# Kernel optimization log

Hardware: AMD Instinct MI355X
Metric: run time of the kernel (lower is better)

Reference implementation:

```python
import jax, jax.numpy as jnp
from jax import lax
import numpy as np

WIN = 7            # skimage structural_similarity default win_size
K1, K2 = 0.01, 0.03
DATA_RANGE = 1.0


def _mean_filter_valid(x, win):
    k = jnp.ones((1, 1, win, win), x.dtype) / (win * win)
    y = lax.conv_general_dilated(x[:, None], k, (1, 1), 'VALID')
    return y[:, 0]


def ssim_loss(img1, img2):
    # img1, img2: (B, H, W); skimage-style SSIM, mean over batch of (1 - ssim)
    f = lambda z: _mean_filter_valid(z, WIN)
    NP = WIN * WIN
    cov_norm = NP / (NP - 1.0)  # unbiased estimator, as in skimage
    ux, uy = f(img1), f(img2)
    uxx, uyy, uxy = f(img1 * img1), f(img2 * img2), f(img1 * img2)
    vx = cov_norm * (uxx - ux * ux)
    vy = cov_norm * (uyy - uy * uy)
    vxy = cov_norm * (uxy - ux * uy)
    C1 = (K1 * DATA_RANGE) ** 2
    C2 = (K2 * DATA_RANGE) ** 2
    S = ((2 * ux * uy + C1) * (2 * vxy + C2)) / ((ux * ux + uy * uy + C1) * (vx + vy + C2))
    return jnp.mean(1.0 - jnp.mean(S, axis=(1, 2)))


def conv2d_same(x, w, b):
    # x: (B, Cin, H, W), w: (Cout, Cin, 3, 3)
    y = lax.conv_general_dilated(x, w, (1, 1), 'SAME')
    return y + b[None, :, None, None]


def maxpool2(x):
    return lax.reduce_window(x, -jnp.inf, lax.max, (1, 1, 2, 2), (1, 1, 2, 2), 'VALID')


def features(x, w1, b1, w2, b2, w3, b3, w4, b4):
    h = jax.nn.relu(conv2d_same(x, w1, b1))
    h = jax.nn.relu(conv2d_same(h, w2, b2))
    h = maxpool2(h)
    h = jax.nn.relu(conv2d_same(h, w3, b3))
    h = jax.nn.relu(conv2d_same(h, w4, b4))
    return h


def _conv_init(key, cout, cin, k=3):
    # torch Conv2d default init: U(-s, s), s = 1/sqrt(cin*k*k)
    kw, kb = jax.random.split(key)
    s = 1.0 / np.sqrt(cin * k * k)
    w = jax.random.uniform(kw, (cout, cin, k, k), jnp.float32, -s, s)
    b = jax.random.uniform(kb, (cout,), jnp.float32, -s, s)
    return w, b


def setup_inputs() -> dict:
    key = jax.random.key(0)
    ks = jax.random.split(key, 6)
    B, H, W = 8, 256, 256
    sr = jax.random.uniform(ks[0], (B, 1, H, W), jnp.float32)
    hr = jax.random.uniform(ks[1], (B, 1, H, W), jnp.float32)
    w1, b1 = _conv_init(ks[2], 64, 1)
    w2, b2 = _conv_init(ks[3], 128, 64)
    w3, b3 = _conv_init(ks[4], 256, 128)
    w4, b4 = _conv_init(ks[5], 256, 256)
    return {"sr": sr, "hr": hr, "w1": w1, "b1": b1, "w2": w2, "b2": b2,
            "w3": w3, "b3": b3, "w4": w4, "b4": b4}


def reference(sr, hr, w1, b1, w2, b2, w3, b3, w4, b4):
    mse_weight, ssim_weight, perceptual_weight = 1.0, 0.5, 0.1
    mse = jnp.mean((sr - hr) ** 2)
    # torch detaches before SSIM (numpy round-trip) -> no gradient through SSIM
    ssim_l = ssim_loss(lax.stop_gradient(sr[:, 0]), lax.stop_gradient(hr[:, 0]))
    sr_f = features(sr, w1, b1, w2, b2, w3, b3, w4, b4)
    hr_f = features(hr, w1, b1, w2, b2, w3, b3, w4, b4)
    perceptual = jnp.mean((sr_f - hr_f) ** 2)
    total = mse_weight * mse + ssim_weight * ssim_l + perceptual_weight * perceptual
    return total, mse, ssim_l, perceptual
```

## Files before the change

kernel.cpp:

```cpp
#include <hip/hip_runtime.h>
#include <hip/hip_bf16.h>

typedef __hip_bfloat16 bf16;
typedef unsigned char u8;
typedef __attribute__((ext_vector_type(4))) float f32x4;
typedef __attribute__((ext_vector_type(8))) int i32x8;
typedef __attribute__((ext_vector_type(4))) unsigned int u32x4;

struct L4 { long a, b, c, d; };
struct U2 { u32x4 x, y; };

typedef __attribute__((address_space(3))) unsigned int lds_uint;
typedef __attribute__((address_space(1))) const unsigned int g_uint;
__device__ inline void gload_lds16(const void* g, void* l) {
    __builtin_amdgcn_global_load_lds((g_uint*)g, (lds_uint*)l, 16, 0, 0);
}

__device__ inline void block_reduce_atomic(float v, float* dst) {
    #pragma unroll
    for (int o = 32; o > 0; o >>= 1) v += __shfl_down(v, o, 64);
    __shared__ float ws[8];
    const int lane = threadIdx.x & 63;
    const int wid  = threadIdx.x >> 6;
    if (lane == 0) ws[wid] = v;
    __syncthreads();
    if (threadIdx.x == 0) {
        float s = 0.f;
        const int nw = (blockDim.x + 63) >> 6;
        for (int i = 0; i < nw; ++i) s += ws[i];
        atomicAdd(dst, s);
    }
}

__global__ void prep_loss_kernel(
    const float* __restrict__ w2, u8* __restrict__ wb2,
    const float* __restrict__ w3, u8* __restrict__ wb3,
    const float* __restrict__ w4, u8* __restrict__ wb4,
    const float* __restrict__ x, const float* __restrict__ y,
    float* __restrict__ accs) {
    const int blk = blockIdx.x;
    if (blk < 3744) {
        const float* w; u8* wb; int CIN, CO, idx;
        if (blk < 288)       { w = w2; wb = wb2; CIN = 64;  CO = 128; idx = blk * 256 + threadIdx.x; }
        else if (blk < 1440) { w = w3; wb = wb3; CIN = 128; CO = 256; idx = (blk - 288) * 256 + threadIdx.x; }
        else                 { w = w4; wb = wb4; CIN = 256; CO = 256; idx = (blk - 1440) * 256 + threadIdx.x; }
        int n = CO * 9 * CIN;
        if (idx >= n) return;
        int t = idx % 9;
        int rest = idx / 9;
        int ci = rest % CIN;
        int co = rest / CIN;
        float v = w[idx];
        int p = ci >> 5, c32 = ci & 31;
        size_t off = (size_t)p * 288 * CO;
        if (t < 8) off += (((size_t)t * 2 + (c32 >> 4)) * CO + co) * 16 + (c32 & 15);
        else       off += 256 * (size_t)CO + (((size_t)(c32 >> 4)) * CO + co) * 16 + (c32 & 15);
        int r = __builtin_amdgcn_cvt_pk_fp8_f32(v, v, 0, false);
        wb[off] = (u8)(r & 0xff);
        return;
    }
    const int lb = blk - 3744;
    float val = 0.f;
    float* dst;
    if (lb < 1960) {
        dst = accs + 1;
        const int b = lb / 245;
        const int t = (lb - b * 245) * 256 + threadIdx.x;
        if (t < 250 * 250) {
            const int i = t / 250, j = t - (t / 250) * 250;
            const float* xp = x + (size_t)b * 65536;
            const float* yp = y + (size_t)b * 65536;
            float sx = 0.f, sy = 0.f, sxx = 0.f, syy = 0.f, sxy = 0.f;
            #pragma unroll
            for (int dy = 0; dy < 7; ++dy) {
                const float* xr = xp + (size_t)(i + dy) * 256 + j;
                const float* yr = yp + (size_t)(i + dy) * 256 + j;
                #pragma unroll
                for (int dx = 0; dx < 7; ++dx) {
                    float a = xr[dx], c = yr[dx];
                    sx += a; sy += c;
                    sxx += a * a; syy += c * c; sxy += a * c;
                }
            }
            const float inv = 1.f / 49.f;
            const float cn  = 49.f / 48.f;
            float ux = sx * inv, uy = sy * inv;
            float vx  = cn * (sxx * inv - ux * ux);
            float vy  = cn * (syy * inv - uy * uy);
            float vxy = cn * (sxy * inv - ux * uy);
            const float C1 = 1e-4f, C2 = 9e-4f;
            val = ((2.f * ux * uy + C1) * (2.f * vxy + C2)) /
                  ((ux * ux + uy * uy + C1) * (vx + vy + C2));
        }
    } else {
        dst = accs + 0;
        int i = (lb - 1960) * 256 + threadIdx.x;
        float4 a = ((const float4*)x)[i];
        float4 b = ((const float4*)y)[i];
        float d0 = a.x - b.x, d1 = a.y - b.y, d2 = a.z - b.z, d3 = a.w - b.w;
        val = d0 * d0 + d1 * d1 + d2 * d2 + d3 * d3;
    }
    block_reduce_atomic(val, dst);
}

__global__ void finalize_kernel(const float* __restrict__ accs, float* __restrict__ out) {
    if (threadIdx.x == 0) {
        float mse    = accs[0] * (1.f / 524288.f);
        float ssim_l = 1.f - accs[1] * (1.f / 500000.f);
        float perc   = accs[2] * (1.f / 33554432.f);
        out[0] = mse + 0.5f * ssim_l + 0.1f * perc;
        out[1] = mse;
        out[2] = ssim_l;
        out[3] = perc;
    }
}

__global__ __launch_bounds__(256) void conv1_kernel(
    const float* __restrict__ sr, const float* __restrict__ hr, int nb, int b0,
    const float* __restrict__ w, const float* __restrict__ bias,
    u8* __restrict__ out) {
    const int H = 256, W = 256;
    const int img = blockIdx.y;
    const float* in = (img < nb) ? (sr + (size_t)(b0 + img) * 65536)
                                 : (hr + (size_t)(b0 + img - nb) * 65536);
    int px = blockIdx.x * 256 + threadIdx.x;
    int y = px >> 8, x = px & 255;
    float p[9];
    #pragma unroll
    for (int dy = 0; dy < 3; ++dy)
        #pragma unroll
        for (int dx = 0; dx < 3; ++dx) {
            int gy = y + dy - 1, gx = x + dx - 1;
            float v = 0.f;
            if ((unsigned)gy < (unsigned)H && (unsigned)gx < (unsigned)W)
                v = in[(size_t)gy * W + gx];
            p[dy * 3 + dx] = v;
        }
    #pragma unroll
    for (int g = 0; g < 8; ++g) {
        float v[8];
        #pragma unroll
        for (int c = 0; c < 8; ++c) {
            int co = g * 8 + c;
            float a = bias[co];
            #pragma unroll
            for (int k = 0; k < 9; ++k) a += w[co * 9 + k] * p[k];
            v[c] = fmaxf(a, 0.f);
        }
        uint2 o;
        int r;
        r = __builtin_amdgcn_cvt_pk_fp8_f32(v[0], v[1], 0, false);
        o.x = __builtin_amdgcn_cvt_pk_fp8_f32(v[2], v[3], r, true);
        r = __builtin_amdgcn_cvt_pk_fp8_f32(v[4], v[5], 0, false);
        o.y = __builtin_amdgcn_cvt_pk_fp8_f32(v[6], v[7], r, true);
        *(uint2*)(out + (((size_t)img * 8 + g) * 65536 + px) * 8) = o;
    }
}

#define BUF_SZ   32768
#define N_ACT_CH 720
#define N_CHUNK  1872
#define WT_BOFF  11520

__global__ __launch_bounds__(256, 2) void conv2_ss(
    const u8* __restrict__ in, const u8* __restrict__ wb,
    const float* __restrict__ bias, u8* __restrict__ out,
    const float* __restrict__ zbuf) {
    const int H = 256, W = 256, CO = 128;
    const size_t HW = 65536;
    const int tid  = threadIdx.x;
    const int lane = tid & 63;
    const int wn   = tid >> 6;
    const int xl = lane & 15;
    const int kq = lane >> 4;
    const int x0 = blockIdx.x * 16;
    const int y0 = blockIdx.y * 16;
    const int img = blockIdx.z >> 1;
    const int co0 = (blockIdx.z & 1) << 6;

    __shared__ __align__(16) char smem[59904];

    f32x4 acc[4][4];
    #pragma unroll
    for (int m = 0; m < 4; ++m)
        #pragma unroll
        for (int n = 0; n < 4; ++n) acc[m][n] = (f32x4){0.f, 0.f, 0.f, 0.f};

    const u8* inp = in + (size_t)img * 8 * HW * 8;

    {
        char* d = smem + tid * 16;
        #pragma unroll
        for (int i = 0; i < 15; ++i) {
            int c = tid + i * 256;
            if (c >= 2 * N_CHUNK) break;
            int ph = (c >= N_CHUNK) ? 1 : 0;
            int c2 = c - ph * N_CHUNK;
            const char* src = (const char*)zbuf;
            if (c2 < N_ACT_CH) {
                int g = c2 / 180, r = c2 - g * 180;
                int row = r / 10, pp = r - row * 10;
                int gy = y0 - 1 + row, colb = x0 - 2 + pp * 2;
                if ((unsigned)gy < (unsigned)H && (unsigned)colb < (unsigned)(W - 1))
                    src = (const char*)(inp + (((size_t)(g + ph * 4)) * HW +
                                              (size_t)gy * W + colb) * 8);
            } else {
                int c3 = c2 - N_ACT_CH;
                size_t o;
                if (c3 < 1024) {
                    int gt = c3 >> 6, co = c3 & 63;
                    o = ((size_t)gt * CO + co0 + co) * 16;
                } else {
                    int c4 = c3 - 1024;
                    int q = c4 >> 6, co = c4 & 63;
                    o = 256 * (size_t)CO + ((size_t)q * CO + co0 + co) * 16;
                }
                src = (const char*)(wb + (size_t)ph * 288 * CO + o);
            }
            gload_lds16(src, d + i * 4096);
        }
    }

    int mxo[2];
    #pragma unroll
    for (int g = 0; g < 2; ++g) {
        int t = g * 4 + kq;
        int dy = t / 3, dx = t - dy * 3;
        mxo[g] = (dy * 20 + dx) * 8;
    }
    const int abase = ((wn * 4) * 20 + xl + 1) * 8;
    const int awmx  = WT_BOFF + kq * 2048 + xl * 16;
    const int aw8   = WT_BOFF + 16384 + (kq >> 1) * 1024 + xl * 16 + (kq & 1) * 8;
    const int ab8   = kq * 2880 + abase + (2 * 20 + 2) * 8;

    __syncthreads();

    #pragma unroll
    for (int p = 0; p < 2; ++p) {
        const char* base = smem + p * 29952;
        #pragma unroll
        for (int g = 0; g < 2; ++g) {
            i32x8 A[4];
            #pragma unroll
            for (int mt = 0; mt < 4; ++mt) {
                const char* pa = base + awmx + g * 8192 + mt * 256;
                U2 u{*(const u32x4*)pa, *(const u32x4*)(pa + 1024)};
                A[mt] = __builtin_bit_cast(i32x8, u);
            }
            #pragma unroll
            for (int nt = 0; nt < 4; ++nt) {
                const char* pb = base + abase + mxo[g] + nt * 160;
                L4 l{*(const long*)pb, *(const long*)(pb + 2880),
                     *(const long*)(pb + 5760), *(const long*)(pb + 8640)};
                i32x8 B = __builtin_bit_cast(i32x8, l);
                #pragma unroll
                for (int mt = 0; mt < 4; ++mt)
                    acc[mt][nt] = __builtin_amdgcn_mfma_scale_f32_16x16x128_f8f6f4(
                        A[mt], B, acc[mt][nt], 0, 0,
                        0, 0x7F7F7F7F, 0, 0x7F7F7F7F);
            }
        }
        {
            long A8[4], B8[4];
            #pragma unroll
            for (int mt = 0; mt < 4; ++mt)
                A8[mt] = *(const long*)(base + aw8 + mt * 256);
            #pragma unroll
            for (int nt = 0; nt < 4; ++nt)
                B8[nt] = *(const long*)(base + ab8 + nt * 160);
            #pragma unroll
            for (int mt = 0; mt < 4; ++mt)
                #pragma unroll
                for (int nt = 0; nt < 4; ++nt)
                    acc[mt][nt] = __builtin_amdgcn_mfma_f32_16x16x32_fp8_fp8(
                        A8[mt], B8[nt], acc[mt][nt], 0, 0, 0);
        }
    }

    const int Hp = H >> 1, Wp = W >> 1;
    const size_t HWp = (size_t)Hp * Wp;
    #pragma unroll
    for (int j = 0; j < 2; ++j) {
        const int py = (y0 + wn * 4 + 2 * j) >> 1;
        const int px = (x0 + xl) >> 1;
        #pragma unroll
        for (int mt = 0; mt < 4; ++mt) {
            const int cb = co0 + mt * 16 + kq * 4;
            const f32x4 bv = *(const f32x4*)(bias + cb);
            float v[4];
            #pragma unroll
            for (int r = 0; r < 4; ++r) {
                float a = acc[mt][2 * j][r] + bv[r];
                float b = acc[mt][2 * j + 1][r] + bv[r];
                float m = fmaxf(a, b);
                m = fmaxf(m, __shfl_xor(m, 1));
                v[r] = fmaxf(m, 0.f);
            }
            if (!(lane & 1)) {
                int w0 = __builtin_amdgcn_cvt_pk_fp8_f32(v[0], v[1], 0, false);
                w0 = __builtin_amdgcn_cvt_pk_fp8_f32(v[2], v[3], w0, true);
                *(int*)(out + (((size_t)img * (CO >> 3) + (cb >> 3)) * HWp +
                               (size_t)py * Wp + px) * 8 + (cb & 7)) = w0;
            }
        }
    }
}

template <int CIN, int EPI>
__global__ __launch_bounds__(256, 2) void conv_mx(
    const u8* __restrict__ in, const u8* __restrict__ wb,
    const float* __restrict__ bias, u8* __restrict__ out,
    int H, int W, int CO,
    const float* __restrict__ zbuf) {
    const int tid  = threadIdx.x;
    const int lane = tid & 63;
    const int wn   = tid >> 6;
    const int xl = lane & 15;
    const int kq = lane >> 4;
    const int x0 = blockIdx.x * 16;
    const int y0 = blockIdx.y * 16;
    const int ngrp = CO >> 6;
    const int img = blockIdx.z / ngrp;
    const int co0 = (blockIdx.z - img * ngrp) << 6;

    __shared__ __align__(16) char smem[2 * BUF_SZ];

    f32x4 acc[4][4];
    #pragma unroll
    for (int m = 0; m < 4; ++m)
        #pragma unroll
        for (int n = 0; n < 4; ++n) acc[m][n] = (f32x4){0.f, 0.f, 0.f, 0.f};

    const size_t HW = (size_t)H * W;
    const u8* inp = in + (size_t)img * (CIN >> 3) * HW * 8;

    const char* srcp[8];
    long adv[8];
    #pragma unroll
    for (int i = 0; i < 8; ++i) {
        int c = tid + i * 256;
        srcp[i] = (const char*)zbuf;
        adv[i] = 0;
        if (c < N_ACT_CH) {
            int g = c / 180, r = c - g * 180;
            int row = r / 10, pp = r - row * 10;
            int gy = y0 - 1 + row, colb = x0 - 2 + pp * 2;
            if ((unsigned)gy < (unsigned)H && (unsigned)colb < (unsigned)(W - 1)) {
                srcp[i] = (const char*)(inp + ((size_t)g * HW + (size_t)gy * W + colb) * 8);
                adv[i] = 4 * HW * 8;
            }
        } else if (c < N_CHUNK) {
            int c2 = c - N_ACT_CH;
            size_t o;
            if (c2 < 1024) {
                int gt = c2 >> 6, co = c2 & 63;
                o = ((size_t)gt * CO + co0 + co) * 16;
            } else {
                int c3 = c2 - 1024;
                int q = c3 >> 6, co = c3 & 63;
                o = 256 * (size_t)CO + ((size_t)q * CO + co0 + co) * 16;
            }
            srcp[i] = (const char*)(wb + o);
            adv[i] = 288 * (size_t)CO;
        }
    }

    int mxo[2];
    #pragma unroll
    for (int g = 0; g < 2; ++g) {
        int t = g * 4 + kq;
        int dy = t / 3, dx = t - dy * 3;
        mxo[g] = (dy * 20 + dx) * 8;
    }
    const int abase = ((wn * 4) * 20 + xl + 1) * 8;
    const int awmx  = WT_BOFF + kq * 2048 + xl * 16;
    const int aw8   = WT_BOFF + 16384 + (kq >> 1) * 1024 + xl * 16 + (kq & 1) * 8;
    const int ab8   = kq * 2880 + abase + (2 * 20 + 2) * 8;

    const int P = CIN / 32;

    {
        char* d = smem + tid * 16;
        #pragma unroll
        for (int i = 0; i < 8; ++i) {
            gload_lds16(srcp[i], d + i * 4096);
            srcp[i] += adv[i];
        }
    }

    for (int p = 0; p < P; ++p) {
        __syncthreads();
        if (p + 1 < P) {
            char* d = smem + ((p + 1) & 1) * BUF_SZ + tid * 16;
            #pragma unroll
            for (int i = 0; i < 8; ++i) {
                gload_lds16(srcp[i], d + i * 4096);
                srcp[i] += adv[i];
            }
        }
        const char* base = smem + (p & 1) * BUF_SZ;
        #pragma unroll
        for (int g = 0; g < 2; ++g) {
            i32x8 A[4];
            #pragma unroll
            for (int mt = 0; mt < 4; ++mt) {
                const char* pa = base + awmx + g * 8192 + mt * 256;
                U2 u{*(const u32x4*)pa, *(const u32x4*)(pa + 1024)};
                A[mt] = __builtin_bit_cast(i32x8, u);
            }
            #pragma unroll
            for (int nt = 0; nt < 4; ++nt) {
                const char* pb = base + abase + mxo[g] + nt * 160;
                L4 l{*(const long*)pb, *(const long*)(pb + 2880),
                     *(const long*)(pb + 5760), *(const long*)(pb + 8640)};
                i32x8 B = __builtin_bit_cast(i32x8, l);
                #pragma unroll
                for (int mt = 0; mt < 4; ++mt)
                    acc[mt][nt] = __builtin_amdgcn_mfma_scale_f32_16x16x128_f8f6f4(
                        A[mt], B, acc[mt][nt], 0, 0,
                        0, 0x7F7F7F7F, 0, 0x7F7F7F7F);
            }
        }
        {
            long A8[4], B8[4];
            #pragma unroll
            for (int mt = 0; mt < 4; ++mt)
                A8[mt] = *(const long*)(base + aw8 + mt * 256);
            #pragma unroll
            for (int nt = 0; nt < 4; ++nt)
                B8[nt] = *(const long*)(base + ab8 + nt * 160);
            #pragma unroll
            for (int mt = 0; mt < 4; ++mt)
                #pragma unroll
                for (int nt = 0; nt < 4; ++nt)
                    acc[mt][nt] = __builtin_amdgcn_mfma_f32_16x16x32_fp8_fp8(
                        A8[mt], B8[nt], acc[mt][nt], 0, 0, 0);
        }
    }

    #pragma unroll
    for (int nt = 0; nt < 4; ++nt) {
        const int y = y0 + wn * 4 + nt;
        #pragma unroll
        for (int mt = 0; mt < 4; ++mt) {
            const int cb = co0 + mt * 16 + kq * 4;
            const f32x4 bv = *(const f32x4*)(bias + cb);
            float v[4];
            #pragma unroll
            for (int r = 0; r < 4; ++r) v[r] = fmaxf(acc[mt][nt][r] + bv[r], 0.f);
            int w0 = __builtin_amdgcn_cvt_pk_fp8_f32(v[0], v[1], 0, false);
            w0 = __builtin_amdgcn_cvt_pk_fp8_f32(v[2], v[3], w0, true);
            *(int*)(out + (((size_t)img * (CO >> 4) + (cb >> 4)) * HW +
                           (size_t)y * W + x0 + xl) * 16 + (cb & 15)) = w0;
        }
    }
}

#define C4_ACT  10368
#define C4_WT   20736
#define C4_BUF  39168
#define C4_NCH  2448

__global__ __launch_bounds__(256, 2) void conv4_fused(
    const char* __restrict__ wsb,
    unsigned aOff,
    unsigned wOff,
    unsigned zOff,
    const float* __restrict__ bias,
    unsigned hrOff,
    float* __restrict__ pacc) {
    const int tid  = threadIdx.x;
    const int lane = tid & 63;
    const int wn   = tid >> 6;
    const int xl = lane & 15;
    const int kq = lane >> 4;
    const int x0 = blockIdx.x * 16;
    const int y0 = blockIdx.y * 16;
    const int img = blockIdx.z >> 2;
    const int co0 = (blockIdx.z & 3) << 6;

    __shared__ __align__(16) char smem[2 * C4_BUF];

    f32x4 accS[4][4], accH[4][4];
    #pragma unroll
    for (int m = 0; m < 4; ++m)
        #pragma unroll
        for (int n = 0; n < 4; ++n) {
            accS[m][n] = (f32x4){0.f, 0.f, 0.f, 0.f};
            accH[m][n] = (f32x4){0.f, 0.f, 0.f, 0.f};
        }

    const unsigned inoff = aOff + (unsigned)img * 4194304u;

    unsigned off[10];
    #pragma unroll
    for (int i = 0; i < 10; ++i) {
        int c = tid + i * 256;
        off[i] = zOff;
        if (c < 1296) {
            int c2 = (c >= 648) ? c - 648 : c;
            int g2 = c2 / 324, rem = c2 - g2 * 324;
            int row = rem / 18, col = rem - row * 18;
            int gy = y0 - 1 + row, gx = x0 - 1 + col;
            if ((unsigned)gy < 128u && (unsigned)gx < 128u)
                off[i] = inoff + ((c >= 648) ? hrOff : 0u) +
                         (unsigned)((g2 * 16384 + gy * 128 + gx) * 16);
        } else if (c < C4_NCH) {
            int c3 = c - 1296;
            unsigned o;
            if (c3 < 1024) {
                int kblk = c3 >> 6, co = c3 & 63;
                o = (unsigned)((kblk * 256 + co0 + co) * 16);
            } else {
                int c4 = c3 - 1024;
                int h = c4 >> 6, co = c4 & 63;
                o = 65536u + (unsigned)((h * 256 + co0 + co) * 16);
            }
            off[i] = wOff + o;
        }
    }

    int bmx[2];
    #pragma unroll
    for (int g = 0; g < 2; ++g) {
        int t = g * 4 + kq;
        int dy = t / 3, dx = t - dy * 3;
        bmx[g] = (dy * 18 + dx) * 16;
    }
    const int bnt0 = ((wn * 4) * 18 + xl) * 16;
    const int awmx = C4_WT + kq * 2048 + xl * 16;
    const int aw8  = C4_WT + 16384 + (kq >> 1) * 1024 + xl * 16 + (kq & 1) * 8;
    const int ab8  = ((wn * 4 + 2) * 18 + xl + 2) * 16 +
                     (kq >> 1) * 5184 + (kq & 1) * 8;

#define C4_STAGE(DB) do {                                                   \
        char* d_ = (DB) + tid * 16;                                         \
        _Pragma("unroll")                                                   \
        for (int i_ = 0; i_ < 10; ++i_) {                                   \
            if (i_ < 9 || tid < 144) {                                      \
                gload_lds16(wsb + off[i_], d_ + i_ * 4096);                 \
                if (i_ < 5 || (i_ == 5 && tid < 16)) {                      \
                    if (off[i_] != zOff) off[i_] += 524288u;                \
                } else {                                                    \
                    off[i_] += 73728u;                                      \
                }                                                           \
            }                                                               \
        } } while (0)

    C4_STAGE(smem);

    for (int pp = 0; pp < 8; ++pp) {
        __syncthreads();
        if (pp < 7) C4_STAGE(smem + ((pp + 1) & 1) * C4_BUF);
        const char* base = smem + (pp & 1) * C4_BUF;
        const char* aS = base;
        const char* aH = base + C4_ACT;
        #pragma unroll
        for (int g = 0; g < 2; ++g) {
            i32x8 A[4];
            #pragma unroll
            for (int mt = 0; mt < 4; ++mt) {
                const char* pa = base + awmx + g * 8192 + mt * 256;
                U2 u{*(const u32x4*)pa, *(const u32x4*)(pa + 1024)};
                A[mt] = __builtin_bit_cast(i32x8, u);
            }
            #pragma unroll
            for (int nt = 0; nt < 4; ++nt) {
                const int bo = bnt0 + nt * 288 + bmx[g];
                U2 us{*(const u32x4*)(aS + bo), *(const u32x4*)(aS + bo + 5184)};
                i32x8 BS = __builtin_bit_cast(i32x8, us);
                #pragma unroll
                for (int mt = 0; mt < 4; ++mt)
                    accS[mt][nt] = __builtin_amdgcn_mfma_scale_f32_16x16x128_f8f6f4(
                        A[mt], BS, accS[mt][nt], 0, 0,
                        0, 0x7F7F7F7F, 0, 0x7F7F7F7F);
                U2 uh{*(const u32x4*)(aH + bo), *(const u32x4*)(aH + bo + 5184)};
                i32x8 BH = __builtin_bit_cast(i32x8, uh);
                #pragma unroll
                for (int mt = 0; mt < 4; ++mt)
                    accH[mt][nt] = __builtin_amdgcn_mfma_scale_f32_16x16x128_f8f6f4(
                        A[mt], BH, accH[mt][nt], 0, 0,
                        0, 0x7F7F7F7F, 0, 0x7F7F7F7F);
            }
        }
        {
            long A8[4];
            #pragma unroll
            for (int mt = 0; mt < 4; ++mt)
                A8[mt] = *(const long*)(base + aw8 + mt * 256);
            #pragma unroll
            for (int nt = 0; nt < 4; ++nt) {
                long bs = *(const long*)(aS + ab8 + nt * 288);
                long bh = *(const long*)(aH + ab8 + nt * 288);
                #pragma unroll
                for (int mt = 0; mt < 4; ++mt) {
                    accS[mt][nt] = __builtin_amdgcn_mfma_f32_16x16x32_fp8_fp8(
                        A8[mt], bs, accS[mt][nt], 0, 0, 0);
                    accH[mt][nt] = __builtin_amdgcn_mfma_f32_16x16x32_fp8_fp8(
                        A8[mt], bh, accH[mt][nt], 0, 0, 0);
                }
            }
        }
    }
#undef C4_STAGE

    float s = 0.f;
    #pragma unroll
    for (int mt = 0; mt < 4; ++mt) {
        const int cb = co0 + mt * 16 + kq * 4;
        const f32x4 bv = *(const f32x4*)(bias + cb);
        #pragma unroll
        for (int nt = 0; nt < 4; ++nt) {
            #pragma unroll
            for (int r = 0; r < 4; ++r) {
                float vs = fmaxf(accS[mt][nt][r] + bv[r], 0.f);
                float vh = fmaxf(accH[mt][nt][r] + bv[r], 0.f);
                float d = vs - vh;
                s += d * d;
            }
        }
    }
    #pragma unroll
    for (int o = 32; o > 0; o >>= 1) s += __shfl_down(s, o, 64);
    __syncthreads();
    if (lane == 0) *(float*)(smem + wn * 4) = s;
    __syncthreads();
    if (tid == 0) {
        float tot = *(float*)(smem) + *(float*)(smem + 4) +
                    *(float*)(smem + 8) + *(float*)(smem + 12);
        atomicAdd(pacc, tot);
    }
}

extern "C" void kernel_launch(void* const* d_in, const int* in_sizes, int n_in,
                              void* d_out, int out_size, void* d_ws, size_t ws_size,
                              hipStream_t stream) {
    const float* sr = (const float*)d_in[0];
    const float* hr = (const float*)d_in[1];
    const float* w1 = (const float*)d_in[2];
    const float* b1 = (const float*)d_in[3];
    const float* w2 = (const float*)d_in[4];
    const float* b2 = (const float*)d_in[5];
    const float* w3 = (const float*)d_in[6];
    const float* b3 = (const float*)d_in[7];
    const float* w4 = (const float*)d_in[8];
    const float* b4 = (const float*)d_in[9];
    float* out = (float*)d_out;

    char* ws = (char*)d_ws;
    size_t off = 0;
    float* accs = (float*)(ws + off); off += 256;
    float* zbuf = (float*)(ws + off); off += 256;
    u8* wb2 = (u8*)(ws + off); off += (size_t)128 * 9 * 64;
    u8* wb3 = (u8*)(ws + off); off += (size_t)256 * 9 * 128;
    u8* wb4 = (u8*)(ws + off); off += (size_t)256 * 9 * 256;
    const size_t fixed = (off + 255) & ~(size_t)255;

    const size_t MB = 1024u * 1024u;
    int nb = 8;
    while (nb > 1 && fixed + (size_t)nb * 12 * MB > ws_size) nb >>= 1;

    u8* A = (u8*)(ws + fixed);
    u8* P = (u8*)(ws + fixed + (size_t)nb * 8 * MB);

    hipMemsetAsync(ws, 0, 512, stream);
    prep_loss_kernel<<<6216, 256, 0, stream>>>(w2, wb2, w3, wb3, w4, wb4, sr, hr, accs);

    for (int b0 = 0; b0 < 8; b0 += nb) {
        const int ni = 2 * nb;
        conv1_kernel<<<dim3(256, ni), 256, 0, stream>>>(sr, hr, nb, b0, w1, b1, A);
        conv2_ss<<<dim3(16, 16, ni * 2), 256, 0, stream>>>(A, wb2, b2, P, zbuf);
        conv_mx<128, 0><<<dim3(8, 8, ni * 4), 256, 0, stream>>>(
            P, wb3, b3, A, 128, 128, 256, zbuf);
        conv4_fused<<<dim3(8, 8, nb * 4), 256, 0, stream>>>(
            (const char*)ws, (unsigned)fixed,
            (unsigned)((char*)wb4 - ws), (unsigned)((char*)zbuf - ws),
            b4, (unsigned)nb * 4194304u, accs + 2);
    }

    finalize_kernel<<<1, 1, 0, stream>>>(accs, out);
}
```

Baseline: 400.2 us.

## Replace conv3 kernel with templated dual-image fused conv shared with conv4

Drops the separate conv_mx kernel for conv3 and reuses the conv4 kernel as a template (phase count, epilogue, image shift), so each block computes the sr and hr images together and shares every weight tile load between them. conv2's pooled output layout moves from 8-channel to 16-channel groups to match the fused kernel's input format. It also raises wave priority (s_setprio) around the MFMA section. The trade-offs are more accumulator registers per block and half as many blocks for conv3.

```diff
diff --git a/kernel.cpp b/kernel.cpp
--- a/kernel.cpp
+++ b/kernel.cpp
@@ -299,159 +299,9 @@
             if (!(lane & 1)) {
                 int w0 = __builtin_amdgcn_cvt_pk_fp8_f32(v[0], v[1], 0, false);
                 w0 = __builtin_amdgcn_cvt_pk_fp8_f32(v[2], v[3], w0, true);
-                *(int*)(out + (((size_t)img * (CO >> 3) + (cb >> 3)) * HWp +
-                               (size_t)py * Wp + px) * 8 + (cb & 7)) = w0;
-            }
-        }
-    }
-}
-
-template <int CIN, int EPI>
-__global__ __launch_bounds__(256, 2) void conv_mx(
-    const u8* __restrict__ in, const u8* __restrict__ wb,
-    const float* __restrict__ bias, u8* __restrict__ out,
-    int H, int W, int CO,
-    const float* __restrict__ zbuf) {
-    const int tid  = threadIdx.x;
-    const int lane = tid & 63;
-    const int wn   = tid >> 6;
-    const int xl = lane & 15;
-    const int kq = lane >> 4;
-    const int x0 = blockIdx.x * 16;
-    const int y0 = blockIdx.y * 16;
-    const int ngrp = CO >> 6;
-    const int img = blockIdx.z / ngrp;
-    const int co0 = (blockIdx.z - img * ngrp) << 6;
-
-    __shared__ __align__(16) char smem[2 * BUF_SZ];
-
-    f32x4 acc[4][4];
-    #pragma unroll
-    for (int m = 0; m < 4; ++m)
-        #pragma unroll
-        for (int n = 0; n < 4; ++n) acc[m][n] = (f32x4){0.f, 0.f, 0.f, 0.f};
-
-    const size_t HW = (size_t)H * W;
-    const u8* inp = in + (size_t)img * (CIN >> 3) * HW * 8;
-
-    const char* srcp[8];
-    long adv[8];
-    #pragma unroll
-    for (int i = 0; i < 8; ++i) {
-        int c = tid + i * 256;
-        srcp[i] = (const char*)zbuf;
-        adv[i] = 0;
-        if (c < N_ACT_CH) {
-            int g = c / 180, r = c - g * 180;
-            int row = r / 10, pp = r - row * 10;
-            int gy = y0 - 1 + row, colb = x0 - 2 + pp * 2;
-            if ((unsigned)gy < (unsigned)H && (unsigned)colb < (unsigned)(W - 1)) {
-                srcp[i] = (const char*)(inp + ((size_t)g * HW + (size_t)gy * W + colb) * 8);
-                adv[i] = 4 * HW * 8;
-            }
-        } else if (c < N_CHUNK) {
-            int c2 = c - N_ACT_CH;
-            size_t o;
-            if (c2 < 1024) {
-                int gt = c2 >> 6, co = c2 & 63;
-                o = ((size_t)gt * CO + co0 + co) * 16;
-            } else {
-                int c3 = c2 - 1024;
-                int q = c3 >> 6, co = c3 & 63;
-                o = 256 * (size_t)CO + ((size_t)q * CO + co0 + co) * 16;
-            }
-            srcp[i] = (const char*)(wb + o);
-            adv[i] = 288 * (size_t)CO;
-        }
-    }
-
-    int mxo[2];
-    #pragma unroll
-    for (int g = 0; g < 2; ++g) {
-        int t = g * 4 + kq;
-        int dy = t / 3, dx = t - dy * 3;
-        mxo[g] = (dy * 20 + dx) * 8;
-    }
-    const int abase = ((wn * 4) * 20 + xl + 1) * 8;
-    const int awmx  = WT_BOFF + kq * 2048 + xl * 16;
-    const int aw8   = WT_BOFF + 16384 + (kq >> 1) * 1024 + xl * 16 + (kq & 1) * 8;
-    const int ab8   = kq * 2880 + abase + (2 * 20 + 2) * 8;
-
-    const int P = CIN / 32;
-
-    {
-        char* d = smem + tid * 16;
-        #pragma unroll
-        for (int i = 0; i < 8; ++i) {
-            gload_lds16(srcp[i], d + i * 4096);
-            srcp[i] += adv[i];
-        }
-    }
-
-    for (int p = 0; p < P; ++p) {
-        __syncthreads();
-        if (p + 1 < P) {
-            char* d = smem + ((p + 1) & 1) * BUF_SZ + tid * 16;
-            #pragma unroll
-            for (int i = 0; i < 8; ++i) {
-                gload_lds16(srcp[i], d + i * 4096);
-                srcp[i] += adv[i];
-            }
-        }
-        const char* base = smem + (p & 1) * BUF_SZ;
-        #pragma unroll
-        for (int g = 0; g < 2; ++g) {
-            i32x8 A[4];
-            #pragma unroll
-            for (int mt = 0; mt < 4; ++mt) {
-                const char* pa = base + awmx + g * 8192 + mt * 256;
-                U2 u{*(const u32x4*)pa, *(const u32x4*)(pa + 1024)};
-                A[mt] = __builtin_bit_cast(i32x8, u);
-            }
-            #pragma unroll
-            for (int nt = 0; nt < 4; ++nt) {
-                const char* pb = base + abase + mxo[g] + nt * 160;
-                L4 l{*(const long*)pb, *(const long*)(pb + 2880),
-                     *(const long*)(pb + 5760), *(const long*)(pb + 8640)};
-                i32x8 B = __builtin_bit_cast(i32x8, l);
-                #pragma unroll
-                for (int mt = 0; mt < 4; ++mt)
-                    acc[mt][nt] = __builtin_amdgcn_mfma_scale_f32_16x16x128_f8f6f4(
-                        A[mt], B, acc[mt][nt], 0, 0,
-                        0, 0x7F7F7F7F, 0, 0x7F7F7F7F);
-            }
-        }
-        {
-            long A8[4], B8[4];
-            #pragma unroll
-            for (int mt = 0; mt < 4; ++mt)
-                A8[mt] = *(const long*)(base + aw8 + mt * 256);
-            #pragma unroll
-            for (int nt = 0; nt < 4; ++nt)
-                B8[nt] = *(const long*)(base + ab8 + nt * 160);
-            #pragma unroll
-            for (int mt = 0; mt < 4; ++mt)
-                #pragma unroll
-                for (int nt = 0; nt < 4; ++nt)
-                    acc[mt][nt] = __builtin_amdgcn_mfma_f32_16x16x32_fp8_fp8(
-                        A8[mt], B8[nt], acc[mt][nt], 0, 0, 0);
-        }
-    }
-
-    #pragma unroll
-    for (int nt = 0; nt < 4; ++nt) {
-        const int y = y0 + wn * 4 + nt;
-        #pragma unroll
-        for (int mt = 0; mt < 4; ++mt) {
-            const int cb = co0 + mt * 16 + kq * 4;
-            const f32x4 bv = *(const f32x4*)(bias + cb);
-            float v[4];
-            #pragma unroll
-            for (int r = 0; r < 4; ++r) v[r] = fmaxf(acc[mt][nt][r] + bv[r], 0.f);
-            int w0 = __builtin_amdgcn_cvt_pk_fp8_f32(v[0], v[1], 0, false);
-            w0 = __builtin_amdgcn_cvt_pk_fp8_f32(v[2], v[3], w0, true);
-            *(int*)(out + (((size_t)img * (CO >> 4) + (cb >> 4)) * HW +
-                           (size_t)y * W + x0 + xl) * 16 + (cb & 15)) = w0;
+                *(int*)(out + (((size_t)img * (CO >> 4) + (cb >> 4)) * HWp +
+                               (size_t)py * Wp + px) * 16 + (cb & 15)) = w0;
+            }
         }
     }
 }
@@ -461,13 +311,16 @@
 #define C4_BUF  39168
 #define C4_NCH  2448
 
-__global__ __launch_bounds__(256, 2) void conv4_fused(
-    const char* __restrict__ wsb,
-    unsigned aOff,
+template <int NPH, int EPI, int IMGSH>
+__global__ __launch_bounds__(256, 2) void conv34_fused(
+    char* __restrict__ wsb,
+    unsigned inOff,
     unsigned wOff,
     unsigned zOff,
     const float* __restrict__ bias,
-    unsigned hrOff,
+    unsigned inHrOff,
+    unsigned outOff,
+    unsigned outHrOff,
     float* __restrict__ pacc) {
     const int tid  = threadIdx.x;
     const int lane = tid & 63;
@@ -490,7 +343,7 @@
             accH[m][n] = (f32x4){0.f, 0.f, 0.f, 0.f};
         }
 
-    const unsigned inoff = aOff + (unsigned)img * 4194304u;
+    const unsigned inoff = inOff + ((unsigned)img << IMGSH);
 
     unsigned off[10];
     #pragma unroll
@@ -503,7 +356,7 @@
             int row = rem / 18, col = rem - row * 18;
             int gy = y0 - 1 + row, gx = x0 - 1 + col;
             if ((unsigned)gy < 128u && (unsigned)gx < 128u)
-                off[i] = inoff + ((c >= 648) ? hrOff : 0u) +
+                off[i] = inoff + ((c >= 648) ? inHrOff : 0u) +
                          (unsigned)((g2 * 16384 + gy * 128 + gx) * 16);
         } else if (c < C4_NCH) {
             int c3 = c - 1296;
@@ -549,12 +402,13 @@
 
     C4_STAGE(smem);
 
-    for (int pp = 0; pp < 8; ++pp) {
+    for (int pp = 0; pp < NPH; ++pp) {
         __syncthreads();
-        if (pp < 7) C4_STAGE(smem + ((pp + 1) & 1) * C4_BUF);
+        if (pp < NPH - 1) C4_STAGE(smem + ((pp + 1) & 1) * C4_BUF);
         const char* base = smem + (pp & 1) * C4_BUF;
         const char* aS = base;
         const char* aH = base + C4_ACT;
+        __builtin_amdgcn_s_setprio(1);
         #pragma unroll
         for (int g = 0; g < 2; ++g) {
             i32x8 A[4];
@@ -601,34 +455,60 @@
                 }
             }
         }
+        __builtin_amdgcn_s_setprio(0);
     }
 #undef C4_STAGE
 
-    float s = 0.f;
-    #pragma unroll
-    for (int mt = 0; mt < 4; ++mt) {
-        const int cb = co0 + mt * 16 + kq * 4;
-        const f32x4 bv = *(const f32x4*)(bias + cb);
+    if (EPI == 0) {
         #pragma unroll
         for (int nt = 0; nt < 4; ++nt) {
-            #pragma unroll
-            for (int r = 0; r < 4; ++r) {
-                float vs = fmaxf(accS[mt][nt][r] + bv[r], 0.f);
-                float vh = fmaxf(accH[mt][nt][r] + bv[r], 0.f);
-                float d = vs - vh;
-                s += d * d;
-            }
-        }
-    }
-    #pragma unroll
-    for (int o = 32; o > 0; o >>= 1) s += __shfl_down(s, o, 64);
-    __syncthreads();
-    if (lane == 0) *(float*)(smem + wn * 4) = s;
-    __syncthreads();
-    if (tid == 0) {
-        float tot = *(float*)(smem) + *(float*)(smem + 4) +
-                    *(float*)(smem + 8) + *(float*)(smem + 12);
-        atomicAdd(pacc, tot);
+            const int y = y0 + wn * 4 + nt;
+            #pragma unroll
+            for (int mt = 0; mt < 4; ++mt) {
+                const int cb = co0 + mt * 16 + kq * 4;
+                const f32x4 bv = *(const f32x4*)(bias + cb);
+                const unsigned po = (unsigned)(((cb >> 4) * 16384 +
+                                    y * 128 + x0 + xl) * 16 + (cb & 15));
+                float v[4];
+                #pragma unroll
+                for (int r = 0; r < 4; ++r) v[r] = fmaxf(accS[mt][nt][r] + bv[r], 0.f);
+                int w0 = __builtin_amdgcn_cvt_pk_fp8_f32(v[0], v[1], 0, false);
+                w0 = __builtin_amdgcn_cvt_pk_fp8_f32(v[2], v[3], w0, true);
+                *(int*)(wsb + outOff + ((unsigned)img << 22) + po) = w0;
+                #pragma unroll
+                for (int r = 0; r < 4; ++r) v[r] = fmaxf(accH[mt][nt][r] + bv[r], 0.f);
+                w0 = __builtin_amdgcn_cvt_pk_fp8_f32(v[0], v[1], 0, false);
+                w0 = __builtin_amdgcn_cvt_pk_fp8_f32(v[2], v[3], w0, true);
+                *(int*)(wsb + outOff + outHrOff + ((unsigned)img << 22) + po) = w0;
+            }
+        }
+    } else {
+        float s = 0.f;
+        #pragma unroll
+        for (int mt = 0; mt < 4; ++mt) {
+            const int cb = co0 + mt * 16 + kq * 4;
+            const f32x4 bv = *(const f32x4*)(bias + cb);
+            #pragma unroll
+            for (int nt = 0; nt < 4; ++nt) {
+                #pragma unroll
+                for (int r = 0; r < 4; ++r) {
+                    float vs = fmaxf(accS[mt][nt][r] + bv[r], 0.f);
+                    float vh = fmaxf(accH[mt][nt][r] + bv[r], 0.f);
+                    float d = vs - vh;
+                    s += d * d;
+                }
+            }
+        }
+        #pragma unroll
+        for (int o = 32; o > 0; o >>= 1) s += __shfl_down(s, o, 64);
+        __syncthreads();
+        if (lane == 0) *(float*)(smem + wn * 4) = s;
+        __syncthreads();
+        if (tid == 0) {
+            float tot = *(float*)(smem) + *(float*)(smem + 4) +
+                        *(float*)(smem + 8) + *(float*)(smem + 12);
+            atomicAdd(pacc, tot);
+        }
     }
 }
 
@@ -663,6 +543,10 @@
     u8* A = (u8*)(ws + fixed);
     u8* P = (u8*)(ws + fixed + (size_t)nb * 8 * MB);
 
+    const unsigned zOffU = (unsigned)((char*)zbuf - ws);
+    const unsigned aOffU = (unsigned)fixed;
+    const unsigned pOffU = (unsigned)(fixed + (size_t)nb * 8 * MB);
+
     hipMemsetAsync(ws, 0, 512, stream);
     prep_loss_kernel<<<6216, 256, 0, stream>>>(w2, wb2, w3, wb3, w4, wb4, sr, hr, accs);
 
@@ -670,12 +554,12 @@
         const int ni = 2 * nb;
         conv1_kernel<<<dim3(256, ni), 256, 0, stream>>>(sr, hr, nb, b0, w1, b1, A);
         conv2_ss<<<dim3(16, 16, ni * 2), 256, 0, stream>>>(A, wb2, b2, P, zbuf);
-        conv_mx<128, 0><<<dim3(8, 8, ni * 4), 256, 0, stream>>>(
-            P, wb3, b3, A, 128, 128, 256, zbuf);
-        conv4_fused<<<dim3(8, 8, nb * 4), 256, 0, stream>>>(
-            (const char*)ws, (unsigned)fixed,
-            (unsigned)((char*)wb4 - ws), (unsigned)((char*)zbuf - ws),
-            b4, (unsigned)nb * 4194304u, accs + 2);
+        conv34_fused<4, 0, 21><<<dim3(8, 8, nb * 4), 256, 0, stream>>>(
+            ws, pOffU, (unsigned)((char*)wb3 - ws), zOffU, b3,
+            (unsigned)nb << 21, aOffU, (unsigned)nb << 22, nullptr);
+        conv34_fused<8, 1, 22><<<dim3(8, 8, nb * 4), 256, 0, stream>>>(
+            ws, aOffU, (unsigned)((char*)wb4 - ws), zOffU, b4,
+            (unsigned)nb << 22, 0u, 0u, accs + 2);
     }
 
     finalize_kernel<<<1, 1, 0, stream>>>(accs, out);
```

Result: faster. 387.3 us (-3.2%).
